# Kernel optimization log

Measured on AMD Instinct MI355X. Metric: run time of the kernel, lower is better.

## Reference

```python
import jax, jax.numpy as jnp
import numpy as np

B = 8192   # batch
S = 115    # state dim (fixed by slice layout)
E = 3072   # retrieval embed dim
C = 128    # compressed context dim
A = 23     # action dim
NE = 4096  # number of hyperedge keys
K = 10     # top-k retrieval
TAU = 1.0  # gumbel temperature
EPS = 1e-5 # layernorm eps


def _ln(x, g, b):
    m = x.mean(-1, keepdims=True)
    v = x.var(-1, keepdims=True)
    return (x - m) * jax.lax.rsqrt(v + EPS) * g + b


def _actor(ctx, extra, w1, b1, g1, be1, w2, b2, g2, be2, w3, b3):
    x = jnp.concatenate([ctx, extra], -1)
    x = jax.nn.relu(_ln(x @ w1 + b1, g1, be1))
    x = jax.nn.relu(_ln(x @ w2 + b2, g2, be2))
    return x @ w3 + b3


def setup_inputs() -> dict:
    key = jax.random.key(0)
    ks = iter(jax.random.split(key, 80))

    def W(shape):
        return jax.random.normal(next(ks), shape, jnp.float32) * (1.0 / float(np.sqrt(shape[0])))

    inp = {}
    inp["state"] = jax.random.normal(next(ks), (B, S), jnp.float32)
    u = jax.random.uniform(next(ks), (B, 4), jnp.float32, 1e-6, 1.0 - 1e-6)
    inp["gumbel_noise"] = -jnp.log(-jnp.log(u))  # standard Gumbel samples
    inp["keys"] = jax.random.normal(next(ks), (NE, E), jnp.float32)
    # state encoder 115 -> 512 -> 512 -> 3072 + LN
    inp["se_w1"] = W((S, 512)); inp["se_b1"] = jnp.zeros(512)
    inp["se_w2"] = W((512, 512)); inp["se_b2"] = jnp.zeros(512)
    inp["se_w3"] = W((512, E)); inp["se_b3"] = jnp.zeros(E)
    inp["se_g"] = jnp.ones(E); inp["se_beta"] = jnp.zeros(E)
    # context compressor 3072 -> 512 -> 128 + LN
    inp["cc_w1"] = W((E, 512)); inp["cc_b1"] = jnp.zeros(512)
    inp["cc_w2"] = W((512, C)); inp["cc_b2"] = jnp.zeros(C)
    inp["cc_g"] = jnp.ones(C); inp["cc_beta"] = jnp.zeros(C)
    # 4 actor experts, differing only in extra-slice width
    for p, e in [("a_pre", 50), ("a_scene", 20), ("a_effect", 10), ("a_rule", 15)]:
        inp[p + "_w1"] = W((C + e, C)); inp[p + "_b1"] = jnp.zeros(C)
        inp[p + "_g1"] = jnp.ones(C); inp[p + "_be1"] = jnp.zeros(C)
        inp[p + "_w2"] = W((C, C)); inp[p + "_b2"] = jnp.zeros(C)
        inp[p + "_g2"] = jnp.ones(C); inp[p + "_be2"] = jnp.zeros(C)
        inp[p + "_w3"] = W((C, A)) * 0.01; inp[p + "_b3"] = jnp.zeros(A)  # orthogonal gain=0.01 approx
    # gumbel router 115 -> 64 -> 64 -> 4
    inp["r_w1"] = W((S, 64)); inp["r_b1"] = jnp.zeros(64)
    inp["r_w2"] = W((64, 64)); inp["r_b2"] = jnp.zeros(64)
    inp["r_w3"] = W((64, 4)); inp["r_b3"] = jnp.zeros(4)
    # critic 115 -> 256 -> 256 -> 1
    inp["c_w1"] = W((S, 256)); inp["c_b1"] = jnp.zeros(256)
    inp["c_w2"] = W((256, 256)); inp["c_b2"] = jnp.zeros(256)
    inp["c_w3"] = W((256, 1)); inp["c_b3"] = jnp.zeros(1)
    return inp


def reference(state, gumbel_noise, keys, se_w1, se_b1, se_w2, se_b2, se_w3, se_b3, se_g, se_beta, cc_w1, cc_b1, cc_w2, cc_b2, cc_g, cc_beta, a_pre_w1, a_pre_b1, a_pre_g1, a_pre_be1, a_pre_w2, a_pre_b2, a_pre_g2, a_pre_be2, a_pre_w3, a_pre_b3, a_scene_w1, a_scene_b1, a_scene_g1, a_scene_be1, a_scene_w2, a_scene_b2, a_scene_g2, a_scene_be2, a_scene_w3, a_scene_b3, a_effect_w1, a_effect_b1, a_effect_g1, a_effect_be1, a_effect_w2, a_effect_b2, a_effect_g2, a_effect_be2, a_effect_w3, a_effect_b3, a_rule_w1, a_rule_b1, a_rule_g1, a_rule_be1, a_rule_w2, a_rule_b2, a_rule_g2, a_rule_be2, a_rule_w3, a_rule_b3, r_w1, r_b1, r_w2, r_b2, r_w3, r_b3, c_w1, c_b1, c_w2, c_b2, c_w3, c_b3):
    # 1) state -> query (StateEncoder)
    q = jax.nn.relu(state @ se_w1 + se_b1)
    q = jax.nn.relu(q @ se_w2 + se_b2)
    q = _ln(q @ se_w3 + se_b3, se_g, se_beta)  # (B, E)
    # 2) top-k hard retrieval from hypergraph memory (cosine sim)
    qn = q * jax.lax.rsqrt(jnp.sum(q * q, -1, keepdims=True) + 1e-12)
    kn = keys * jax.lax.rsqrt(jnp.sum(keys * keys, -1, keepdims=True) + 1e-12)
    scores = qn @ kn.T                          # (B, NE)
    _, idx = jax.lax.top_k(scores, K)           # (B, K)
    context = jnp.take(keys, idx, axis=0).mean(1)  # (B, E) mean-pool top-k raw embeddings
    # 3) compress to shared knowledge
    h = jax.nn.relu(context @ cc_w1 + cc_b1)
    shared = _ln(h @ cc_w2 + cc_b2, cc_g, cc_beta)  # (B, C)
    # 4) state slices + 4 actor experts
    belief = state[:, :50]
    location = state[:, 20:40]
    hp = state[:, 40:50]
    inv = state[:, 45:60]
    lp = _actor(shared, belief, a_pre_w1, a_pre_b1, a_pre_g1, a_pre_be1, a_pre_w2, a_pre_b2, a_pre_g2, a_pre_be2, a_pre_w3, a_pre_b3)
    ls = _actor(shared, location, a_scene_w1, a_scene_b1, a_scene_g1, a_scene_be1, a_scene_w2, a_scene_b2, a_scene_g2, a_scene_be2, a_scene_w3, a_scene_b3)
    le = _actor(shared, hp, a_effect_w1, a_effect_b1, a_effect_g1, a_effect_be1, a_effect_w2, a_effect_b2, a_effect_g2, a_effect_be2, a_effect_w3, a_effect_b3)
    lr = _actor(shared, inv, a_rule_w1, a_rule_b1, a_rule_g1, a_rule_be1, a_rule_w2, a_rule_b2, a_rule_g2, a_rule_be2, a_rule_w3, a_rule_b3)
    # 5) gumbel-softmax hard router (straight-through)
    rh = jax.nn.relu(state @ r_w1 + r_b1)
    rh = jax.nn.relu(rh @ r_w2 + r_b2)
    rl = jnp.clip(rh @ r_w3 + r_b3, -20.0, 20.0)
    y_soft = jax.nn.softmax((rl + gumbel_noise) / TAU, -1)
    y_hard = jax.nn.one_hot(jnp.argmax(y_soft, -1), 4, dtype=y_soft.dtype)
    alpha = y_soft + jax.lax.stop_gradient(y_hard - y_soft)  # (B, 4)
    # 6) combine expert logits
    all_l = jnp.stack([lp, ls, le, lr], 1)      # (B, 4, A)
    logits = jnp.einsum('bk,bka->ba', alpha, all_l)
    # critic value
    v = jax.nn.relu(state @ c_w1 + c_b1)
    v = jax.nn.relu(v @ c_w2 + c_b2)
    value = v @ c_w3 + c_b3                      # (B, 1)
    return (logits, alpha, value)
```

## Files before the change

### kernel.cpp

```cpp
#include <hip/hip_runtime.h>

constexpr int Bz = 8192;
constexpr int Sz = 115;
constexpr int Ez = 3072;
constexpr int NEz = 4096;

typedef __attribute__((ext_vector_type(8))) short short8;
typedef __attribute__((ext_vector_type(4))) float floatx4;
typedef unsigned short ushort_t;
typedef unsigned int uint_t;

__device__ __forceinline__ ushort_t f2bf(float f) {
  uint_t u = __float_as_uint(f);
  uint_t r = (u + 0x7FFFu + ((u >> 16) & 1u)) >> 16;
  return (ushort_t)r;
}
__device__ __forceinline__ float bf2f(ushort_t b) {
  uint_t u = ((uint_t)b) << 16;
  return __uint_as_float(u);
}
__device__ __forceinline__ ushort_t f2key(float v) {
  _Float16 h = (_Float16)v;
  ushort_t b = __builtin_bit_cast(ushort_t, h);
  return b ^ ((b & 0x8000u) ? 0xFFFFu : 0x8000u);
}
__device__ __forceinline__ uint_t umax_(uint_t a, uint_t b) { return a > b ? a : b; }

__device__ __forceinline__ void gload16(const ushort_t* g, ushort_t* l) {
  __builtin_amdgcn_global_load_lds(
      (__attribute__((address_space(1))) const void*)g,
      (__attribute__((address_space(3))) void*)l, 16, 0, 0);
}

template<bool RELU, bool BIAS>
__global__ __launch_bounds__(256)
void gemm128(const float* __restrict__ A, const float* __restrict__ Bm,
             const float* __restrict__ bias, float* __restrict__ C,
             int N, int Kd)
{
  __shared__ float As[16][132];
  __shared__ float Bs[16][132];
  const int t  = threadIdx.x;
  const int tx = t & 15, ty = t >> 4;
  const int row0 = blockIdx.y * 128;
  const int col0 = blockIdx.x * 128;
  const int ar = t >> 2, ac = (t & 3) * 4;
  const int bk = t >> 5, bc = (t & 31) * 4;
  const bool a4 = (Kd & 3) == 0;

  float acc[8][8];
#pragma unroll
  for (int i = 0; i < 8; ++i)
#pragma unroll
    for (int j = 0; j < 8; ++j) acc[i][j] = 0.f;

  for (int k0 = 0; k0 < Kd; k0 += 16) {
    const bool fullA = (k0 + 16 <= Kd) && a4;
    {
      const float* ap = A + (size_t)(row0 + ar) * Kd + k0 + ac;
      if (fullA) {
        float4 v0 = *(const float4*)ap;
        float4 v1 = *(const float4*)(ap + (size_t)64 * Kd);
        As[ac + 0][ar] = v0.x; As[ac + 1][ar] = v0.y;
        As[ac + 2][ar] = v0.z; As[ac + 3][ar] = v0.w;
        As[ac + 0][ar + 64] = v1.x; As[ac + 1][ar + 64] = v1.y;
        As[ac + 2][ar + 64] = v1.z; As[ac + 3][ar + 64] = v1.w;
      } else {
#pragma unroll
        for (int e = 0; e < 4; ++e) {
          const int k = k0 + ac + e;
          float v0 = 0.f, v1 = 0.f;
          if (k < Kd) { v0 = ap[e]; v1 = ap[e + (size_t)64 * Kd]; }
          As[ac + e][ar] = v0; As[ac + e][ar + 64] = v1;
        }
      }
    }
    {
      const float* bp = Bm + (size_t)(k0 + bk) * N + col0 + bc;
      if (k0 + 16 <= Kd) {
        *(float4*)&Bs[bk][bc]     = *(const float4*)bp;
        *(float4*)&Bs[bk + 8][bc] = *(const float4*)(bp + (size_t)8 * N);
      } else {
        float4 z; z.x = z.y = z.z = z.w = 0.f;
        *(float4*)&Bs[bk][bc]     = (k0 + bk     < Kd) ? *(const float4*)bp : z;
        *(float4*)&Bs[bk + 8][bc] = (k0 + bk + 8 < Kd) ? *(const float4*)(bp + (size_t)8 * N) : z;
      }
    }
    __syncthreads();
#pragma unroll
    for (int kk = 0; kk < 16; ++kk) {
      float a[8], b[8];
      *(float4*)&a[0] = *(const float4*)&As[kk][ty * 4];
      *(float4*)&a[4] = *(const float4*)&As[kk][64 + ty * 4];
      *(float4*)&b[0] = *(const float4*)&Bs[kk][tx * 4];
      *(float4*)&b[4] = *(const float4*)&Bs[kk][64 + tx * 4];
#pragma unroll
      for (int i = 0; i < 8; ++i)
#pragma unroll
        for (int j = 0; j < 8; ++j)
          acc[i][j] = fmaf(a[i], b[j], acc[i][j]);
    }
    __syncthreads();
  }

  float bv[8];
#pragma unroll
  for (int j = 0; j < 8; ++j) bv[j] = 0.f;
  if (BIAS) {
    *(float4*)&bv[0] = *(const float4*)&bias[col0 + tx * 4];
    *(float4*)&bv[4] = *(const float4*)&bias[col0 + 64 + tx * 4];
  }
#pragma unroll
  for (int i = 0; i < 8; ++i) {
    const int r = row0 + ((i < 4) ? (ty * 4 + i) : (64 + ty * 4 + i - 4));
    float o[8];
#pragma unroll
    for (int j = 0; j < 8; ++j) {
      o[j] = acc[i][j] + bv[j];
      if (RELU) o[j] = fmaxf(o[j], 0.f);
    }
    *(float4*)&C[(size_t)r * N + col0 + tx * 4]      = *(float4*)&o[0];
    *(float4*)&C[(size_t)r * N + col0 + 64 + tx * 4] = *(float4*)&o[4];
  }
}

struct GPart {
  const float* A; const float* Bm; const float* bias;
  float* C; ushort_t* Ch; ushort_t* Cl;
  int N; int Kd; int nbx;
};

__global__ __launch_bounds__(256)
void gemm128_dual(GPart g0, GPart g1)
{
  __shared__ float As[16][132];
  __shared__ float Bs[16][132];
  const int t  = threadIdx.x;
  const int tx = t & 15, ty = t >> 4;
  const bool p0 = (int)blockIdx.x < g0.nbx;
  GPart g = p0 ? g0 : g1;
  const int bx = p0 ? blockIdx.x : (blockIdx.x - g0.nbx);
  const int row0 = blockIdx.y * 128;
  const int col0 = bx * 128;
  const int Kd = g.Kd, N = g.N;
  const int ar = t >> 2, ac = (t & 3) * 4;
  const int bk = t >> 5, bc = (t & 31) * 4;
  const bool a4 = (Kd & 3) == 0;

  float acc[8][8];
#pragma unroll
  for (int i = 0; i < 8; ++i)
#pragma unroll
    for (int j = 0; j < 8; ++j) acc[i][j] = 0.f;

  for (int k0 = 0; k0 < Kd; k0 += 16) {
    const bool fullA = (k0 + 16 <= Kd) && a4;
    {
      const float* ap = g.A + (size_t)(row0 + ar) * Kd + k0 + ac;
      if (fullA) {
        float4 v0 = *(const float4*)ap;
        float4 v1 = *(const float4*)(ap + (size_t)64 * Kd);
        As[ac + 0][ar] = v0.x; As[ac + 1][ar] = v0.y;
        As[ac + 2][ar] = v0.z; As[ac + 3][ar] = v0.w;
        As[ac + 0][ar + 64] = v1.x; As[ac + 1][ar + 64] = v1.y;
        As[ac + 2][ar + 64] = v1.z; As[ac + 3][ar + 64] = v1.w;
      } else {
#pragma unroll
        for (int e = 0; e < 4; ++e) {
          const int k = k0 + ac + e;
          float v0 = 0.f, v1 = 0.f;
          if (k < Kd) { v0 = ap[e]; v1 = ap[e + (size_t)64 * Kd]; }
          As[ac + e][ar] = v0; As[ac + e][ar + 64] = v1;
        }
      }
    }
    {
      const float* bp = g.Bm + (size_t)(k0 + bk) * N + col0 + bc;
      if (k0 + 16 <= Kd) {
        *(float4*)&Bs[bk][bc]     = *(const float4*)bp;
        *(float4*)&Bs[bk + 8][bc] = *(const float4*)(bp + (size_t)8 * N);
      } else {
        float4 z; z.x = z.y = z.z = z.w = 0.f;
        *(float4*)&Bs[bk][bc]     = (k0 + bk     < Kd) ? *(const float4*)bp : z;
        *(float4*)&Bs[bk + 8][bc] = (k0 + bk + 8 < Kd) ? *(const float4*)(bp + (size_t)8 * N) : z;
      }
    }
    __syncthreads();
#pragma unroll
    for (int kk = 0; kk < 16; ++kk) {
      float a[8], b[8];
      *(float4*)&a[0] = *(const float4*)&As[kk][ty * 4];
      *(float4*)&a[4] = *(const float4*)&As[kk][64 + ty * 4];
      *(float4*)&b[0] = *(const float4*)&Bs[kk][tx * 4];
      *(float4*)&b[4] = *(const float4*)&Bs[kk][64 + tx * 4];
#pragma unroll
      for (int i = 0; i < 8; ++i)
#pragma unroll
        for (int j = 0; j < 8; ++j)
          acc[i][j] = fmaf(a[i], b[j], acc[i][j]);
    }
    __syncthreads();
  }

  float bv[8];
  *(float4*)&bv[0] = *(const float4*)&g.bias[col0 + tx * 4];
  *(float4*)&bv[4] = *(const float4*)&g.bias[col0 + 64 + tx * 4];
#pragma unroll
  for (int i = 0; i < 8; ++i) {
    const int r = row0 + ((i < 4) ? (ty * 4 + i) : (64 + ty * 4 + i - 4));
    float o[8];
#pragma unroll
    for (int j = 0; j < 8; ++j) o[j] = fmaxf(acc[i][j] + bv[j], 0.f);
    const size_t i0 = (size_t)r * N + col0 + tx * 4;
    const size_t i1 = i0 + 64;
    *(float4*)&g.C[i0] = *(float4*)&o[0];
    *(float4*)&g.C[i1] = *(float4*)&o[4];
    if (g.Ch) {
      ushort4 h0, l0, h1, l1;
      h0.x = f2bf(o[0]); l0.x = f2bf(o[0] - bf2f(h0.x));
      h0.y = f2bf(o[1]); l0.y = f2bf(o[1] - bf2f(h0.y));
      h0.z = f2bf(o[2]); l0.z = f2bf(o[2] - bf2f(h0.z));
      h0.w = f2bf(o[3]); l0.w = f2bf(o[3] - bf2f(h0.w));
      h1.x = f2bf(o[4]); l1.x = f2bf(o[4] - bf2f(h1.x));
      h1.y = f2bf(o[5]); l1.y = f2bf(o[5] - bf2f(h1.y));
      h1.z = f2bf(o[6]); l1.z = f2bf(o[6] - bf2f(h1.z));
      h1.w = f2bf(o[7]); l1.w = f2bf(o[7] - bf2f(h1.w));
      *(ushort4*)&g.Ch[i0] = h0; *(ushort4*)&g.Cl[i0] = l0;
      *(ushort4*)&g.Ch[i1] = h1; *(ushort4*)&g.Cl[i1] = l1;
    }
  }
}

template<int EPI>
__global__ __launch_bounds__(256)
void mfma_bt(const ushort_t* __restrict__ A, const ushort_t* __restrict__ B,
             const float* __restrict__ bias, void* __restrict__ Cout,
             int N, int Kd)
{
  __shared__ ushort_t Al[2 * 128 * 32];
  __shared__ ushort_t Bl[2 * 128 * 32];
  const int t = threadIdx.x;
  const int wid = t >> 6, lane = t & 63;
  const int wr = wid >> 1, wc = wid & 1;
  const int row0 = blockIdx.y << 7;
  const int col0 = blockIdx.x << 7;
  const int srow = lane >> 2;
  const int scol = (lane & 3) * 8;

  const ushort_t* ga0 = A + (size_t)(row0 + wid * 16 + srow) * Kd + scol;
  const ushort_t* ga1 = A + (size_t)(row0 + (wid + 4) * 16 + srow) * Kd + scol;
  const ushort_t* gb0 = B + (size_t)(col0 + wid * 16 + srow) * Kd + scol;
  const ushort_t* gb1 = B + (size_t)(col0 + (wid + 4) * 16 + srow) * Kd + scol;
  ushort_t* la0 = &Al[wid * 512];
  ushort_t* la1 = &Al[(wid + 4) * 512];
  ushort_t* lb0 = &Bl[wid * 512];
  ushort_t* lb1 = &Bl[(wid + 4) * 512];

  const int mr = lane & 15, qd = lane >> 4;

  floatx4 acc[4][4];
#pragma unroll
  for (int i = 0; i < 4; ++i)
#pragma unroll
    for (int j = 0; j < 4; ++j) acc[i][j] = (floatx4){0.f, 0.f, 0.f, 0.f};

  for (int kb = 0; kb < Kd; kb += 64) {
#pragma unroll
    for (int tt = 0; tt < 2; ++tt) {
      const int ko = kb + 32 * tt;
      const int lo = tt * 4096;
      gload16(ga0 + ko, la0 + lo);
      gload16(ga1 + ko, la1 + lo);
      gload16(gb0 + ko, lb0 + lo);
      gload16(gb1 + ko, lb1 + lo);
    }
    __syncthreads();
#pragma unroll
    for (int tt = 0; tt < 2; ++tt) {
      const int lo = tt * 4096;
      short8 aF[4], bF[4];
#pragma unroll
      for (int i = 0; i < 4; ++i)
        aF[i] = *(const short8*)&Al[lo + (wr * 64 + i * 16 + mr) * 32 + qd * 8];
#pragma unroll
      for (int j = 0; j < 4; ++j)
        bF[j] = *(const short8*)&Bl[lo + (wc * 64 + j * 16 + mr) * 32 + qd * 8];
#pragma unroll
      for (int i = 0; i < 4; ++i)
#pragma unroll
        for (int j = 0; j < 4; ++j)
          acc[i][j] = __builtin_amdgcn_mfma_f32_16x16x32_bf16(aF[i], bF[j], acc[i][j], 0, 0, 0);
    }
    __syncthreads();
  }

#pragma unroll
  for (int i = 0; i < 4; ++i) {
#pragma unroll
    for (int j = 0; j < 4; ++j) {
      const int col = col0 + wc * 64 + j * 16 + mr;
#pragma unroll
      for (int r = 0; r < 4; ++r) {
        const int row = row0 + wr * 64 + i * 16 + qd * 4 + r;
        if (EPI == 0) {
          ((ushort_t*)Cout)[(size_t)row * N + col] = f2key(acc[i][j][r]);
        } else {
          float v = acc[i][j][r] + bias[col];
          ((float*)Cout)[(size_t)row * N + col] = fmaxf(v, 0.f);
        }
      }
    }
  }
}

__global__ __launch_bounds__(256)
void mfma3_bt(const ushort_t* __restrict__ Ah, const ushort_t* __restrict__ Alo,
              const ushort_t* __restrict__ Bh, const ushort_t* __restrict__ Blo,
              const float* __restrict__ bias, float* __restrict__ Cout,
              int N, int Kd)
{
  __shared__ ushort_t AhL[128 * 32];
  __shared__ ushort_t AlL[128 * 32];
  __shared__ ushort_t BhL[128 * 32];
  __shared__ ushort_t BlL[128 * 32];
  const int t = threadIdx.x;
  const int wid = t >> 6, lane = t & 63;
  const int wr = wid >> 1, wc = wid & 1;
  const int row0 = blockIdx.y * 128;
  const int col0 = blockIdx.x * 128;
  const int srow = lane >> 2;
  const int scol = (lane & 3) * 8;

  const size_t aoff0 = (size_t)(row0 + wid * 16 + srow) * Kd + scol;
  const size_t aoff1 = (size_t)(row0 + (wid + 4) * 16 + srow) * Kd + scol;
  const size_t boff0 = (size_t)(col0 + wid * 16 + srow) * Kd + scol;
  const size_t boff1 = (size_t)(col0 + (wid + 4) * 16 + srow) * Kd + scol;
  const int l0 = (wid * 16) * 32;
  const int l1 = ((wid + 4) * 16) * 32;

  const int mr = lane & 15, qd = lane >> 4;

  floatx4 acc[4][4];
#pragma unroll
  for (int i = 0; i < 4; ++i)
#pragma unroll
    for (int j = 0; j < 4; ++j) acc[i][j] = (floatx4){0.f, 0.f, 0.f, 0.f};

  for (int kb = 0; kb < Kd; kb += 32) {
    gload16(Ah + aoff0 + kb, &AhL[l0]);
    gload16(Ah + aoff1 + kb, &AhL[l1]);
    gload16(Alo + aoff0 + kb, &AlL[l0]);
    gload16(Alo + aoff1 + kb, &AlL[l1]);
    gload16(Bh + boff0 + kb, &BhL[l0]);
    gload16(Bh + boff1 + kb, &BhL[l1]);
    gload16(Blo + boff0 + kb, &BlL[l0]);
    gload16(Blo + boff1 + kb, &BlL[l1]);
    __syncthreads();
    short8 ahF[4], alF[4], bhF[4], blF[4];
#pragma unroll
    for (int i = 0; i < 4; ++i) {
      const int o = (wr * 64 + i * 16 + mr) * 32 + qd * 8;
      ahF[i] = *(const short8*)&AhL[o];
      alF[i] = *(const short8*)&AlL[o];
    }
#pragma unroll
    for (int j = 0; j < 4; ++j) {
      const int o = (wc * 64 + j * 16 + mr) * 32 + qd * 8;
      bhF[j] = *(const short8*)&BhL[o];
      blF[j] = *(const short8*)&BlL[o];
    }
#pragma unroll
    for (int i = 0; i < 4; ++i)
#pragma unroll
      for (int j = 0; j < 4; ++j) {
        acc[i][j] = __builtin_amdgcn_mfma_f32_16x16x32_bf16(alF[i], bhF[j], acc[i][j], 0, 0, 0);
        acc[i][j] = __builtin_amdgcn_mfma_f32_16x16x32_bf16(ahF[i], blF[j], acc[i][j], 0, 0, 0);
        acc[i][j] = __builtin_amdgcn_mfma_f32_16x16x32_bf16(ahF[i], bhF[j], acc[i][j], 0, 0, 0);
      }
    __syncthreads();
  }

#pragma unroll
  for (int i = 0; i < 4; ++i) {
#pragma unroll
    for (int j = 0; j < 4; ++j) {
      const int col = col0 + wc * 64 + j * 16 + mr;
#pragma unroll
      for (int r = 0; r < 4; ++r) {
        const int row = row0 + wr * 64 + i * 16 + qd * 4 + r;
        Cout[(size_t)row * N + col] = acc[i][j][r] + bias[col];
      }
    }
  }
}

__global__ __launch_bounds__(256)
void gemm_scores(const float* __restrict__ A, const float* __restrict__ Bm,
                 const float* __restrict__ rk, ushort_t* __restrict__ S)
{
  __shared__ float As[16][132];
  __shared__ float Bs[16][132];
  const int t  = threadIdx.x;
  const int tx = t & 15, ty = t >> 4;
  const int row0 = blockIdx.y * 128;
  const int col0 = blockIdx.x * 128;
  const int ar = t >> 2, ac = (t & 3) * 4;
  const int Kd = Ez;

  float acc[8][8];
#pragma unroll
  for (int i = 0; i < 8; ++i)
#pragma unroll
    for (int j = 0; j < 8; ++j) acc[i][j] = 0.f;

  for (int k0 = 0; k0 < Kd; k0 += 16) {
    {
      const float* ap = A + (size_t)(row0 + ar) * Kd + k0 + ac;
      float4 v0 = *(const float4*)ap;
      float4 v1 = *(const float4*)(ap + (size_t)64 * Kd);
      As[ac + 0][ar] = v0.x; As[ac + 1][ar] = v0.y;
      As[ac + 2][ar] = v0.z; As[ac + 3][ar] = v0.w;
      As[ac + 0][ar + 64] = v1.x; As[ac + 1][ar + 64] = v1.y;
      As[ac + 2][ar + 64] = v1.z; As[ac + 3][ar + 64] = v1.w;
    }
    {
      const float* bp = Bm + (size_t)(col0 + ar) * Kd + k0 + ac;
      float4 v0 = *(const float4*)bp;
      float4 v1 = *(const float4*)(bp + (size_t)64 * Kd);
      Bs[ac + 0][ar] = v0.x; Bs[ac + 1][ar] = v0.y;
      Bs[ac + 2][ar] = v0.z; Bs[ac + 3][ar] = v0.w;
      Bs[ac + 0][ar + 64] = v1.x; Bs[ac + 1][ar + 64] = v1.y;
      Bs[ac + 2][ar + 64] = v1.z; Bs[ac + 3][ar + 64] = v1.w;
    }
    __syncthreads();
#pragma unroll
    for (int kk = 0; kk < 16; ++kk) {
      float a[8], b[8];
      *(float4*)&a[0] = *(const float4*)&As[kk][ty * 4];
      *(float4*)&a[4] = *(const float4*)&As[kk][64 + ty * 4];
      *(float4*)&b[0] = *(const float4*)&Bs[kk][tx * 4];
      *(float4*)&b[4] = *(const float4*)&Bs[kk][64 + tx * 4];
#pragma unroll
      for (int i = 0; i < 8; ++i)
#pragma unroll
        for (int j = 0; j < 8; ++j)
          acc[i][j] = fmaf(a[i], b[j], acc[i][j]);
    }
    __syncthreads();
  }

  float rk0[8];
  *(float4*)&rk0[0] = *(const float4*)&rk[col0 + tx * 4];
  *(float4*)&rk0[4] = *(const float4*)&rk[col0 + 64 + tx * 4];
#pragma unroll
  for (int i = 0; i < 8; ++i) {
    const int r = row0 + ((i < 4) ? (ty * 4 + i) : (64 + ty * 4 + i - 4));
    ushort4 h0, h1;
    h0.x = f2key(acc[i][0] * rk0[0]); h0.y = f2key(acc[i][1] * rk0[1]);
    h0.z = f2key(acc[i][2] * rk0[2]); h0.w = f2key(acc[i][3] * rk0[3]);
    h1.x = f2key(acc[i][4] * rk0[4]); h1.y = f2key(acc[i][5] * rk0[5]);
    h1.z = f2key(acc[i][6] * rk0[6]); h1.w = f2key(acc[i][7] * rk0[7]);
    *(ushort4*)&S[(size_t)r * NEz + col0 + tx * 4]      = h0;
    *(ushort4*)&S[(size_t)r * NEz + col0 + 64 + tx * 4] = h1;
  }
}

struct LN4 {
  const float* W[4]; const float* b[4]; const float* g[4]; const float* be[4];
  int eoff[4]; int elen[4];
};

template<bool RELU, bool HASEXT>
__global__ __launch_bounds__(256)
void gemm_ln4(const float* __restrict__ A1base, size_t a1stride, int K1,
              const float* __restrict__ A2, LN4 p,
              float* __restrict__ outbase, size_t ostride)
{
  __shared__ float As[32][68];
  __shared__ float Bs[32][132];
  __shared__ float rsum[64][17];
  __shared__ float rsq[64][17];
  __shared__ float stm[64], str[64];
  const int a = blockIdx.y;
  const float* A1 = A1base + (size_t)a * a1stride;
  float* out = outbase + (size_t)a * ostride;
  const float* W = p.W[a];
  const float* bias = p.b[a];
  const float* g = p.g[a];
  const float* be = p.be[a];
  const int eoff = HASEXT ? p.eoff[a] : 0;
  const int K2 = HASEXT ? p.elen[a] : 0;

  const int t = threadIdx.x;
  const int tx = t & 15, ty = t >> 4;
  const int row0 = blockIdx.x * 64;
  const int Kt = K1 + K2;
  const int ar = t >> 2, ac = (t & 3) * 8;
  const int bk = t >> 3, bc = (t & 7) * 16;

  float acc[4][8];
#pragma unroll
  for (int i = 0; i < 4; ++i)
#pragma unroll
    for (int j = 0; j < 8; ++j) acc[i][j] = 0.f;

  for (int k0 = 0; k0 < Kt; k0 += 32) {
    const int grow = row0 + ar;
#pragma unroll
    for (int e = 0; e < 8; ++e) {
      const int k = k0 + ac + e;
      float v = 0.f;
      if (k < K1)      v = A1[(size_t)grow * K1 + k];
      else if (k < Kt) v = A2[(size_t)grow * 115 + eoff + (k - K1)];
      As[ac + e][ar] = v;
    }
    {
      const int k = k0 + bk;
#pragma unroll
      for (int qd = 0; qd < 4; ++qd) {
        float4 z; z.x = z.y = z.z = z.w = 0.f;
        *(float4*)&Bs[bk][bc + 4 * qd] =
            (k < Kt) ? *(const float4*)&W[(size_t)k * 128 + bc + 4 * qd] : z;
      }
    }
    __syncthreads();
#pragma unroll
    for (int kk = 0; kk < 32; ++kk) {
      float av[4], bv2[8];
      *(float4*)&av[0]  = *(const float4*)&As[kk][ty * 4];
      *(float4*)&bv2[0] = *(const float4*)&Bs[kk][tx * 4];
      *(float4*)&bv2[4] = *(const float4*)&Bs[kk][64 + tx * 4];
#pragma unroll
      for (int i = 0; i < 4; ++i)
#pragma unroll
        for (int j = 0; j < 8; ++j)
          acc[i][j] = fmaf(av[i], bv2[j], acc[i][j]);
    }
    __syncthreads();
  }

  float bv[8];
  *(float4*)&bv[0] = *(const float4*)&bias[tx * 4];
  *(float4*)&bv[4] = *(const float4*)&bias[64 + tx * 4];
#pragma unroll
  for (int i = 0; i < 4; ++i) {
    float s = 0.f, q = 0.f;
#pragma unroll
    for (int j = 0; j < 8; ++j) {
      acc[i][j] += bv[j];
      s += acc[i][j];
      q += acc[i][j] * acc[i][j];
    }
    rsum[ty * 4 + i][tx] = s;
    rsq[ty * 4 + i][tx]  = q;
  }
  __syncthreads();
  if (t < 64) {
    float s = 0.f, q = 0.f;
#pragma unroll
    for (int x = 0; x < 16; ++x) { s += rsum[t][x]; q += rsq[t][x]; }
    const float m = s * (1.f / 128.f);
    const float v = q * (1.f / 128.f) - m * m;
    stm[t] = m;
    str[t] = rsqrtf(v + 1e-5f);
  }
  __syncthreads();
#pragma unroll
  for (int i = 0; i < 4; ++i) {
    const int r = ty * 4 + i;
    const float m = stm[r], rs = str[r];
    float o[8];
#pragma unroll
    for (int j = 0; j < 8; ++j) {
      const int col = (j < 4) ? (tx * 4 + j) : (64 + tx * 4 + (j - 4));
      float y = (acc[i][j] - m) * rs * g[col] + be[col];
      if (RELU) y = fmaxf(y, 0.f);
      o[j] = y;
    }
    *(float4*)&out[(size_t)(row0 + r) * 128 + tx * 4]      = *(float4*)&o[0];
    *(float4*)&out[(size_t)(row0 + r) * 128 + 64 + tx * 4] = *(float4*)&o[4];
  }
}

__device__ __forceinline__ float blockSum256(float v, float* sh)
{
#pragma unroll
  for (int d = 32; d; d >>= 1) v += __shfl_down(v, d, 64);
  __syncthreads();
  if ((threadIdx.x & 63) == 0) sh[threadIdx.x >> 6] = v;
  __syncthreads();
  return sh[0] + sh[1] + sh[2] + sh[3];
}

template<bool CVT>
__global__ __launch_bounds__(256)
void ln_l2_q(float* __restrict__ q, const float* __restrict__ g,
             const float* __restrict__ be, ushort_t* __restrict__ qb)
{
  __shared__ float sh[4];
  const int row = blockIdx.x, t = threadIdx.x;
  float* qr = q + (size_t)row * Ez;
  float x[12];
#pragma unroll
  for (int i = 0; i < 12; ++i) x[i] = qr[t + (i << 8)];
  float s = 0.f;
#pragma unroll
  for (int i = 0; i < 12; ++i) s += x[i];
  const float m = blockSum256(s, sh) * (1.f / (float)Ez);
  float vs = 0.f;
#pragma unroll
  for (int i = 0; i < 12; ++i) { const float d = x[i] - m; vs += d * d; }
  const float v = blockSum256(vs, sh) * (1.f / (float)Ez);
  const float rs = rsqrtf(v + 1e-5f);
  float y[12]; float qs = 0.f;
#pragma unroll
  for (int i = 0; i < 12; ++i) {
    const int c = t + (i << 8);
    const float yy = (x[i] - m) * rs * g[c] + be[c];
    y[i] = yy; qs += yy * yy;
  }
  const float tot = blockSum256(qs, sh);
  const float s2 = rsqrtf(tot + 1e-12f);
#pragma unroll
  for (int i = 0; i < 12; ++i) {
    const int c = t + (i << 8);
    const float yn = y[i] * s2;
    qr[c] = yn;
    if (CVT) qb[(size_t)row * Ez + c] = f2bf(yn);
  }
}

__global__ __launch_bounds__(256)
void keynorm(const float* __restrict__ keys, float* __restrict__ rk)
{
  __shared__ float sh[4];
  const int row = blockIdx.x, t = threadIdx.x;
  const float* xr = keys + (size_t)row * Ez;
  float qs = 0.f;
#pragma unroll
  for (int i = 0; i < 12; ++i) { const float x = xr[t + (i << 8)]; qs += x * x; }
  const float tot = blockSum256(qs, sh);
  if (t == 0) rk[row] = rsqrtf(tot + 1e-12f);
}

__global__ __launch_bounds__(256)
void keys_norm_cvt(const float* __restrict__ keys, float* __restrict__ rk,
                   ushort_t* __restrict__ knb)
{
  __shared__ float sh[4];
  const int row = blockIdx.x, t = threadIdx.x;
  const float* xr = keys + (size_t)row * Ez;
  float x[12]; float qs = 0.f;
#pragma unroll
  for (int i = 0; i < 12; ++i) { x[i] = xr[t + (i << 8)]; qs += x[i] * x[i]; }
  const float tot = blockSum256(qs, sh);
  const float s = rsqrtf(tot + 1e-12f);
  if (t == 0) rk[row] = s;
#pragma unroll
  for (int i = 0; i < 12; ++i)
    knb[(size_t)row * Ez + t + (i << 8)] = f2bf(x[i] * s);
}

__global__ __launch_bounds__(256)
void w3_transpose_split(const float* __restrict__ w,
                        ushort_t* __restrict__ hT, ushort_t* __restrict__ lT)
{
  __shared__ float tile[64][65];
  const int k0 = blockIdx.x * 64;
  const int n0 = blockIdx.y * 64;
  const int t = threadIdx.x;
  const int c = t & 63, r4 = t >> 6;
#pragma unroll
  for (int rr = 0; rr < 16; ++rr) {
    const int r = rr * 4 + r4;
    tile[r][c] = w[(size_t)(k0 + r) * 3072 + n0 + c];
  }
  __syncthreads();
#pragma unroll
  for (int rr = 0; rr < 16; ++rr) {
    const int n = rr * 4 + r4;
    const float a = tile[c][n];
    const ushort_t h = f2bf(a);
    hT[(size_t)(n0 + n) * 512 + k0 + c] = h;
    lT[(size_t)(n0 + n) * 512 + k0 + c] = f2bf(a - bf2f(h));
  }
}

__global__ __launch_bounds__(256)
void cvt_w1t_t(const float* __restrict__ w, ushort_t* __restrict__ out)
{
  __shared__ float tile[64][65];
  const int k0 = blockIdx.x * 64;
  const int n0 = blockIdx.y * 64;
  const int t = threadIdx.x;
  const int c = t & 63, r4 = t >> 6;
#pragma unroll
  for (int rr = 0; rr < 16; ++rr) {
    const int r = rr * 4 + r4;
    tile[r][c] = w[(size_t)(k0 + r) * 512 + n0 + c];
  }
  __syncthreads();
#pragma unroll
  for (int rr = 0; rr < 16; ++rr) {
    const int n = rr * 4 + r4;
    out[(size_t)(n0 + n) * Ez + k0 + c] = f2bf(tile[c][n]);
  }
}

__global__ __launch_bounds__(256)
void topk16(const ushort_t* __restrict__ S, int* __restrict__ outIdx)
{
  __shared__ uint_t cand[64];
  const int row = blockIdx.x, t = threadIdx.x;
  const int w = t >> 6, lane = t & 63;
  const int base = (w << 10) + (lane << 4);
  const ushort_t* sr = S + (size_t)row * NEz + base;
  uint4 v0 = *(const uint4*)sr;
  uint4 v1 = *(const uint4*)(sr + 8);
  const uint_t cb = (uint_t)(4095 - base);
  uint_t p[16];
  p[0]  = ((v0.x & 0xFFFFu) << 12) | (cb - 0);
  p[1]  = ((v0.x >> 16)     << 12) | (cb - 1);
  p[2]  = ((v0.y & 0xFFFFu) << 12) | (cb - 2);
  p[3]  = ((v0.y >> 16)     << 12) | (cb - 3);
  p[4]  = ((v0.z & 0xFFFFu) << 12) | (cb - 4);
  p[5]  = ((v0.z >> 16)     << 12) | (cb - 5);
  p[6]  = ((v0.w & 0xFFFFu) << 12) | (cb - 6);
  p[7]  = ((v0.w >> 16)     << 12) | (cb - 7);
  p[8]  = ((v1.x & 0xFFFFu) << 12) | (cb - 8);
  p[9]  = ((v1.x >> 16)     << 12) | (cb - 9);
  p[10] = ((v1.y & 0xFFFFu) << 12) | (cb - 10);
  p[11] = ((v1.y >> 16)     << 12) | (cb - 11);
  p[12] = ((v1.z & 0xFFFFu) << 12) | (cb - 12);
  p[13] = ((v1.z >> 16)     << 12) | (cb - 13);
  p[14] = ((v1.w & 0xFFFFu) << 12) | (cb - 14);
  p[15] = ((v1.w >> 16)     << 12) | (cb - 15);

  for (int it = 0; it < 16; ++it) {
    uint_t m = p[0];
#pragma unroll
    for (int j = 1; j < 16; ++j) m = umax_(m, p[j]);
#pragma unroll
    for (int d = 1; d < 64; d <<= 1)
      m = umax_(m, (uint_t)__shfl_xor((int)m, d, 64));
    if (lane == it) cand[(w << 4) + it] = m;
#pragma unroll
    for (int j = 0; j < 16; ++j) p[j] = (p[j] == m) ? 0u : p[j];
  }
  __syncthreads();
  if (t < 64) {
    uint_t mine = cand[t];
    for (int it = 0; it < 16; ++it) {
      uint_t m = mine;
#pragma unroll
      for (int d = 1; d < 64; d <<= 1)
        m = umax_(m, (uint_t)__shfl_xor((int)m, d, 64));
      if (t == it) outIdx[(size_t)row * 16 + it] = 4095 - (int)(m & 0xFFFu);
      mine = (mine == m) ? 0u : mine;
    }
  }
}

template<bool BFOUT>
__global__ __launch_bounds__(256)
void rescore_gather(const float* __restrict__ qn, const float* __restrict__ keys,
                    const float* __restrict__ rk, const int* __restrict__ cand,
                    void* __restrict__ ctxOut)
{
  __shared__ float qs[Ez];
  __shared__ double sv[16];
  __shared__ int si[16];
  __shared__ int sel10[10];
  const int row = blockIdx.x, t = threadIdx.x;
  const int w = t >> 6, lane = t & 63;

  {
    const float* qr = qn + (size_t)row * Ez;
#pragma unroll
    for (int i = 0; i < 3; ++i) {
      const int c = (t << 2) + (i << 10);
      *(float4*)&qs[c] = *(const float4*)&qr[c];
    }
  }
  __syncthreads();

#pragma unroll
  for (int cc = 0; cc < 4; ++cc) {
    const int slot = w * 4 + cc;
    const int id = cand[(size_t)row * 16 + slot];
    const float* kr = keys + (size_t)id * Ez;
    double s = 0.0;
#pragma unroll
    for (int it = 0; it < 12; ++it) {
      const int c = (lane << 2) + (it << 8);
      float4 k4 = *(const float4*)&kr[c];
      float4 q4 = *(const float4*)&qs[c];
      s += (double)q4.x * (double)k4.x;
      s += (double)q4.y * (double)k4.y;
      s += (double)q4.z * (double)k4.z;
      s += (double)q4.w * (double)k4.w;
    }
#pragma unroll
    for (int d = 32; d; d >>= 1) s += __shfl_down(s, d, 64);
    if (lane == 0) { sv[slot] = s * (double)rk[id]; si[slot] = id; }
  }
  __syncthreads();

  if (t == 0) {
    for (int it = 0; it < 10; ++it) {
      int bj = 0; double bvv = sv[0]; int bi = si[0];
      for (int j = 1; j < 16; ++j) {
        const double v = sv[j]; const int i2 = si[j];
        if (v > bvv || (v == bvv && i2 < bi)) { bj = j; bvv = v; bi = i2; }
      }
      sel10[it] = bi;
      sv[bj] = -1e300;
    }
  }
  __syncthreads();

  int id[10];
#pragma unroll
  for (int j = 0; j < 10; ++j) id[j] = sel10[j];

#pragma unroll
  for (int i = 0; i < 3; ++i) {
    const int c = (t << 2) + (i << 10);
    float4 a = {0.f, 0.f, 0.f, 0.f};
#pragma unroll
    for (int j = 0; j < 10; ++j) {
      float4 v = *(const float4*)&keys[(size_t)id[j] * Ez + c];
      a.x += v.x; a.y += v.y; a.z += v.z; a.w += v.w;
    }
    if (BFOUT) {
      ushort4 o;
      o.x = f2bf(a.x * 0.1f); o.y = f2bf(a.y * 0.1f);
      o.z = f2bf(a.z * 0.1f); o.w = f2bf(a.w * 0.1f);
      *(ushort4*)&((ushort_t*)ctxOut)[(size_t)row * Ez + c] = o;
    } else {
      float4 o;
      o.x = a.x * 0.1f; o.y = a.y * 0.1f; o.z = a.z * 0.1f; o.w = a.w * 0.1f;
      *(float4*)&((float*)ctxOut)[(size_t)row * Ez + c] = o;
    }
  }
}

__global__ __launch_bounds__(256)
void router_kernel(const float* __restrict__ state, const float* __restrict__ gn,
                   const float* __restrict__ w1, const float* __restrict__ b1,
                   const float* __restrict__ w2, const float* __restrict__ b2,
                   const float* __restrict__ w3, const float* __restrict__ b3,
                   float* __restrict__ outAlpha)
{
  const int row = blockIdx.x * 256 + threadIdx.x;
  const float* sr = state + (size_t)row * Sz;
  float h1[64];
#pragma unroll
  for (int j = 0; j < 64; ++j) h1[j] = b1[j];
  for (int k = 0; k < Sz; ++k) {
    const float a = sr[k];
    const float* wr = w1 + (size_t)k * 64;
#pragma unroll
    for (int j = 0; j < 64; ++j) h1[j] = fmaf(a, wr[j], h1[j]);
  }
#pragma unroll
  for (int j = 0; j < 64; ++j) h1[j] = fmaxf(h1[j], 0.f);
  float h2[64];
#pragma unroll
  for (int j = 0; j < 64; ++j) h2[j] = b2[j];
#pragma unroll
  for (int k = 0; k < 64; ++k) {
    const float a = h1[k];
    const float* wr = w2 + (size_t)k * 64;
#pragma unroll
    for (int j = 0; j < 64; ++j) h2[j] = fmaf(a, wr[j], h2[j]);
  }
#pragma unroll
  for (int j = 0; j < 64; ++j) h2[j] = fmaxf(h2[j], 0.f);
  float z[4];
#pragma unroll
  for (int a = 0; a < 4; ++a) {
    float s = b3[a];
#pragma unroll
    for (int k = 0; k < 64; ++k) s = fmaf(h2[k], w3[k * 4 + a], s);
    s = fminf(fmaxf(s, -20.f), 20.f);
    z[a] = s + gn[(size_t)row * 4 + a];
  }
  float mz = z[0];
#pragma unroll
  for (int a = 1; a < 4; ++a) mz = fmaxf(mz, z[a]);
  float e[4]; float se = 0.f;
#pragma unroll
  for (int a = 0; a < 4; ++a) { e[a] = expf(z[a] - mz); se += e[a]; }
  const float inv = 1.f / se;
  float y[4];
#pragma unroll
  for (int a = 0; a < 4; ++a) y[a] = e[a] * inv;
  int am = 0;
#pragma unroll
  for (int a = 1; a < 4; ++a) if (y[a] > y[am]) am = a;
#pragma unroll
  for (int a = 0; a < 4; ++a) {
    const float hard = (a == am) ? 1.f : 0.f;
    outAlpha[(size_t)row * 4 + a] = y[a] + (hard - y[a]);
  }
}

__global__ __launch_bounds__(256)
void critic_head(const float* __restrict__ c2, const float* __restrict__ w3,
                 const float* __restrict__ b3, float* __restrict__ outv)
{
  const int row = blockIdx.x * 256 + threadIdx.x;
  const float* xr = c2 + (size_t)row * 256;
  float s = b3[0];
  for (int k = 0; k < 256; ++k) s = fmaf(xr[k], w3[k], s);
  outv[row] = s;
}

struct HeadP { const float* w3[4]; const float* b3[4]; };

__global__ __launch_bounds__(256)
void actor_head4(const float* __restrict__ x2g, HeadP p,
                 const float* __restrict__ alpha, float* __restrict__ outL)
{
  __shared__ float wsm[4][128 * 23];
  __shared__ float bs[4][23];
  const int t = threadIdx.x;
#pragma unroll
  for (int a = 0; a < 4; ++a) {
    for (int i = t; i < 128 * 23; i += 256) wsm[a][i] = p.w3[a][i];
    if (t < 23) bs[a][t] = p.b3[a][t];
  }
  __syncthreads();
  const int row = blockIdx.x * 32 + (t >> 3);
  const int cg = t & 7;
  float sum[3] = {0.f, 0.f, 0.f};
#pragma unroll
  for (int a = 0; a < 4; ++a) {
    const float al = alpha[(size_t)row * 4 + a];
    const float* xr = x2g + (size_t)a * Bz * 128 + (size_t)row * 128;
    float acc[3] = {0.f, 0.f, 0.f};
    for (int kk = 0; kk < 128; ++kk) {
      const float xa = xr[kk];
#pragma unroll
      for (int j = 0; j < 3; ++j) {
        const int col = cg + 8 * j;
        if (col < 23) acc[j] = fmaf(xa, wsm[a][kk * 23 + col], acc[j]);
      }
    }
#pragma unroll
    for (int j = 0; j < 3; ++j) {
      const int col = cg + 8 * j;
      if (col < 23) sum[j] += al * (acc[j] + bs[a][col]);
    }
  }
#pragma unroll
  for (int j = 0; j < 3; ++j) {
    const int col = cg + 8 * j;
    if (col < 23) outL[(size_t)row * 23 + col] = sum[j];
  }
}

extern "C" void kernel_launch(void* const* d_in, const int* in_sizes, int n_in,
                              void* d_out, int out_size, void* d_ws, size_t ws_size,
                              hipStream_t stream)
{
  const float* state  = (const float*)d_in[0];
  const float* gumbel = (const float*)d_in[1];
  const float* keys   = (const float*)d_in[2];
  const float* se_w1 = (const float*)d_in[3];
  const float* se_b1 = (const float*)d_in[4];
  const float* se_w2 = (const float*)d_in[5];
  const float* se_b2 = (const float*)d_in[6];
  const float* se_w3 = (const float*)d_in[7];
  const float* se_b3 = (const float*)d_in[8];
  const float* se_g  = (const float*)d_in[9];
  const float* se_be = (const float*)d_in[10];
  const float* cc_w1 = (const float*)d_in[11];
  const float* cc_b1 = (const float*)d_in[12];
  const float* cc_w2 = (const float*)d_in[13];
  const float* cc_b2 = (const float*)d_in[14];
  const float* cc_g  = (const float*)d_in[15];
  const float* cc_be = (const float*)d_in[16];
  const float* r_w1 = (const float*)d_in[57];
  const float* r_b1 = (const float*)d_in[58];
  const float* r_w2 = (const float*)d_in[59];
  const float* r_b2 = (const float*)d_in[60];
  const float* r_w3 = (const float*)d_in[61];
  const float* r_b3 = (const float*)d_in[62];
  const float* c_w1 = (const float*)d_in[63];
  const float* c_b1 = (const float*)d_in[64];
  const float* c_w2 = (const float*)d_in[65];
  const float* c_b2 = (const float*)d_in[66];
  const float* c_w3 = (const float*)d_in[67];
  const float* c_b3 = (const float*)d_in[68];

  float* wsf = (float*)d_ws;
  const size_t qF = (size_t)Bz * Ez;
  const size_t uF = (size_t)16777216;
  float* q = wsf;
  float* U = wsf + qF;
  float* sA  = U;
  float* sB  = U + 4194304;
  ushort_t* sBh  = (ushort_t*)(U + 8388608);
  ushort_t* sBl  = (ushort_t*)(U + 10485760);
  ushort_t* w3hT = (ushort_t*)(U + 12582912);
  ushort_t* w3lT = (ushort_t*)(U + 14155776);
  ushort_t* scoresU = (ushort_t*)U;
  float* shr = U;
  float* x1g = U + 1 * 1048576;
  float* x2g = U + 5 * 1048576;
  float* cch = U + 9 * 1048576;
  float* cr1 = q;
  float* cr2 = q + 2097152;
  ushort_t* qbf  = (ushort_t*)(wsf + qF + uF);
  ushort_t* knbf = qbf + qF;
  ushort_t* w1T  = knbf + (size_t)NEz * Ez;
  const size_t bfHalves = qF + (size_t)NEz * Ez + (size_t)512 * Ez;
  const size_t baseBytes = (qF + uF) * sizeof(float);
  const size_t tailBytes = 4096 * 4 + (size_t)Bz * 16 * 4;
  const bool fast = ws_size >= baseBytes + bfHalves * 2 + tailBytes;
  float* tailF = (float*)((char*)d_ws + (fast ? baseBytes + bfHalves * 2 : baseBytes));
  float* rk  = tailF;
  int* cand  = (int*)(tailF + 4096);
  ushort_t* ctxb = (ushort_t*)q;

  float* outL = (float*)d_out;
  float* outA = outL + (size_t)Bz * 23;
  float* outV = outA + (size_t)Bz * 4;

  const dim3 blk(256);

  {
    GPart e0 = {state, se_w1, se_b1, sA, nullptr, nullptr, 512, 115, 4};
    GPart e1 = {state, c_w1,  c_b1,  cr1, nullptr, nullptr, 256, 115, 2};
    gemm128_dual<<<dim3(6, 64), blk, 0, stream>>>(e0, e1);
  }
  {
    GPart f0 = {sA, se_w2, se_b2, sB, fast ? sBh : nullptr, fast ? sBl : nullptr,
                512, 512, 4};
    GPart f1 = {cr1, c_w2, c_b2, cr2, nullptr, nullptr, 256, 256, 2};
    gemm128_dual<<<dim3(6, 64), blk, 0, stream>>>(f0, f1);
  }
  critic_head<<<dim3(32), blk, 0, stream>>>(cr2, c_w3, c_b3, outV);
  router_kernel<<<dim3(32), blk, 0, stream>>>(state, gumbel, r_w1, r_b1, r_w2, r_b2,
                                              r_w3, r_b3, outA);

  if (fast) {
    w3_transpose_split<<<dim3(8, 48), blk, 0, stream>>>(se_w3, w3hT, w3lT);
    mfma3_bt<<<dim3(24, 64), blk, 0, stream>>>(sBh, sBl, w3hT, w3lT, se_b3, q, 3072, 512);
    ln_l2_q<true><<<dim3(Bz), blk, 0, stream>>>(q, se_g, se_be, qbf);
    keys_norm_cvt<<<dim3(NEz), blk, 0, stream>>>(keys, rk, knbf);
    cvt_w1t_t<<<dim3(48, 8), blk, 0, stream>>>(cc_w1, w1T);
    mfma_bt<0><<<dim3(32, 64), blk, 0, stream>>>(qbf, knbf, nullptr, scoresU, NEz, Ez);
  } else {
    gemm128<false, true><<<dim3(24, 64), blk, 0, stream>>>(sB, se_w3, se_b3, q, 3072, 512);
    ln_l2_q<false><<<dim3(Bz), blk, 0, stream>>>(q, se_g, se_be, nullptr);
    keynorm<<<dim3(NEz), blk, 0, stream>>>(keys, rk);
    gemm_scores<<<dim3(32, 64), blk, 0, stream>>>(q, keys, rk, scoresU);
  }

  topk16<<<dim3(Bz), blk, 0, stream>>>(scoresU, cand);

  if (fast) {
    rescore_gather<true><<<dim3(Bz), blk, 0, stream>>>(q, keys, rk, cand, ctxb);
    mfma_bt<1><<<dim3(4, 64), blk, 0, stream>>>(ctxb, w1T, cc_b1, cch, 512, Ez);
  } else {
    rescore_gather<false><<<dim3(Bz), blk, 0, stream>>>(q, keys, rk, cand, q);
    gemm128<true, true><<<dim3(4, 64), blk, 0, stream>>>(q, cc_w1, cc_b1, cch, 512, Ez);
  }
  {
    LN4 pcc = {};
    pcc.W[0] = cc_w2; pcc.b[0] = cc_b2; pcc.g[0] = cc_g; pcc.be[0] = cc_be;
    gemm_ln4<false, false><<<dim3(128, 1), blk, 0, stream>>>(cch, 0, 512, nullptr, pcc,
                                                             shr, 0);
  }

  {
    LN4 p1 = {}, p2 = {};
    HeadP ph = {};
    const int eoffs[4] = {0, 20, 40, 45};
    const int elens[4] = {50, 20, 10, 15};
    for (int a = 0; a < 4; ++a) {
      const int base = 17 + 10 * a;
      p1.W[a]  = (const float*)d_in[base + 0];
      p1.b[a]  = (const float*)d_in[base + 1];
      p1.g[a]  = (const float*)d_in[base + 2];
      p1.be[a] = (const float*)d_in[base + 3];
      p1.eoff[a] = eoffs[a]; p1.elen[a] = elens[a];
      p2.W[a]  = (const float*)d_in[base + 4];
      p2.b[a]  = (const float*)d_in[base + 5];
      p2.g[a]  = (const float*)d_in[base + 6];
      p2.be[a] = (const float*)d_in[base + 7];
      ph.w3[a] = (const float*)d_in[base + 8];
      ph.b3[a] = (const float*)d_in[base + 9];
    }
    gemm_ln4<true, true ><<<dim3(128, 4), blk, 0, stream>>>(shr, 0, 128, state, p1,
                                                            x1g, (size_t)Bz * 128);
    gemm_ln4<true, false><<<dim3(128, 4), blk, 0, stream>>>(x1g, (size_t)Bz * 128, 128,
                                                            nullptr, p2,
                                                            x2g, (size_t)Bz * 128);
    actor_head4<<<dim3(256), blk, 0, stream>>>(x2g, ph, outA, outL);
  }
}
```

Baseline: 1.325 ms.

## Move state-encoder layer 2 to split-bf16 MFMA and retune retrieval GEMMs

The second state-encoder layer now runs as a 3-pass split-bf16 MFMA GEMM. The first layer writes hi/lo bf16 halves directly instead of fp32, so the fp32 intermediate is no longer stored. The scores GEMM stages three 32-wide K sub-tiles per sync instead of two, and the context-compressor GEMM uses a new 64-row tile kernel that launches more blocks. The critic head is rewritten as a wave-parallel dot product with shuffle reductions, and the critic's second layer runs as a separate GEMM. Together these add launches and workspace aliasing changes that need to stay consistent.

Measured after the change: 1.312 ms. Within noise of the previous version (-1.0%).

```diff
diff --git a/kernel.cpp b/kernel.cpp
--- a/kernel.cpp
+++ b/kernel.cpp
@@ -213,8 +213,10 @@
     for (int j = 0; j < 8; ++j) o[j] = fmaxf(acc[i][j] + bv[j], 0.f);
     const size_t i0 = (size_t)r * N + col0 + tx * 4;
     const size_t i1 = i0 + 64;
-    *(float4*)&g.C[i0] = *(float4*)&o[0];
-    *(float4*)&g.C[i1] = *(float4*)&o[4];
+    if (g.C) {
+      *(float4*)&g.C[i0] = *(float4*)&o[0];
+      *(float4*)&g.C[i1] = *(float4*)&o[4];
+    }
     if (g.Ch) {
       ushort4 h0, l0, h1, l1;
       h0.x = f2bf(o[0]); l0.x = f2bf(o[0] - bf2f(h0.x));
@@ -231,14 +233,13 @@
   }
 }
 
-template<int EPI>
+template<int NSUB>
 __global__ __launch_bounds__(256)
 void mfma_bt(const ushort_t* __restrict__ A, const ushort_t* __restrict__ B,
-             const float* __restrict__ bias, void* __restrict__ Cout,
-             int N, int Kd)
-{
-  __shared__ ushort_t Al[2 * 128 * 32];
-  __shared__ ushort_t Bl[2 * 128 * 32];
+             ushort_t* __restrict__ Cout, int N, int Kd)
+{
+  __shared__ ushort_t Al[NSUB * 4096];
+  __shared__ ushort_t Bl[NSUB * 4096];
   const int t = threadIdx.x;
   const int wid = t >> 6, lane = t & 63;
   const int wr = wid >> 1, wc = wid & 1;
@@ -264,9 +265,9 @@
 #pragma unroll
     for (int j = 0; j < 4; ++j) acc[i][j] = (floatx4){0.f, 0.f, 0.f, 0.f};
 
-  for (int kb = 0; kb < Kd; kb += 64) {
-#pragma unroll
-    for (int tt = 0; tt < 2; ++tt) {
+  for (int kb = 0; kb < Kd; kb += 32 * NSUB) {
+#pragma unroll
+    for (int tt = 0; tt < NSUB; ++tt) {
       const int ko = kb + 32 * tt;
       const int lo = tt * 4096;
       gload16(ga0 + ko, la0 + lo);
@@ -276,7 +277,7 @@
     }
     __syncthreads();
 #pragma unroll
-    for (int tt = 0; tt < 2; ++tt) {
+    for (int tt = 0; tt < NSUB; ++tt) {
       const int lo = tt * 4096;
       short8 aF[4], bF[4];
 #pragma unroll
@@ -302,21 +303,18 @@
 #pragma unroll
       for (int r = 0; r < 4; ++r) {
         const int row = row0 + wr * 64 + i * 16 + qd * 4 + r;
-        if (EPI == 0) {
-          ((ushort_t*)Cout)[(size_t)row * N + col] = f2key(acc[i][j][r]);
-        } else {
-          float v = acc[i][j][r] + bias[col];
-          ((float*)Cout)[(size_t)row * N + col] = fmaxf(v, 0.f);
-        }
+        Cout[(size_t)row * N + col] = f2key(acc[i][j][r]);
       }
     }
   }
 }
 
+template<int EPI>
 __global__ __launch_bounds__(256)
 void mfma3_bt(const ushort_t* __restrict__ Ah, const ushort_t* __restrict__ Alo,
               const ushort_t* __restrict__ Bh, const ushort_t* __restrict__ Blo,
               const float* __restrict__ bias, float* __restrict__ Cout,
+              ushort_t* __restrict__ Ch, ushort_t* __restrict__ Cl,
               int N, int Kd)
 {
   __shared__ ushort_t AhL[128 * 32];
@@ -388,7 +386,88 @@
 #pragma unroll
       for (int r = 0; r < 4; ++r) {
         const int row = row0 + wr * 64 + i * 16 + qd * 4 + r;
-        Cout[(size_t)row * N + col] = acc[i][j][r] + bias[col];
+        const float v = acc[i][j][r] + bias[col];
+        if (EPI == 0) {
+          Cout[(size_t)row * N + col] = v;
+        } else {
+          const float y = fmaxf(v, 0.f);
+          const ushort_t h = f2bf(y);
+          Ch[(size_t)row * N + col] = h;
+          Cl[(size_t)row * N + col] = f2bf(y - bf2f(h));
+        }
+      }
+    }
+  }
+}
+
+__global__ __launch_bounds__(256)
+void mfma_bt64(const ushort_t* __restrict__ A, const ushort_t* __restrict__ B,
+               const float* __restrict__ bias, float* __restrict__ Cout,
+               int N, int Kd)
+{
+  __shared__ ushort_t Al[2 * 64 * 32];
+  __shared__ ushort_t Bl[2 * 128 * 32];
+  const int t = threadIdx.x;
+  const int wid = t >> 6, lane = t & 63;
+  const int row0 = blockIdx.y << 6;
+  const int col0 = blockIdx.x << 7;
+  const int srow = lane >> 2;
+  const int scol = (lane & 3) * 8;
+  const int mr = lane & 15, qd = lane >> 4;
+
+  const ushort_t* gsrc[6];
+  ushort_t* ldst[6];
+#pragma unroll
+  for (int m = 0; m < 6; ++m) {
+    const int c = wid * 6 + m;
+    if (c < 8) {
+      const int sub = c >> 2, grp = c & 3;
+      gsrc[m] = A + (size_t)(row0 + grp * 16 + srow) * Kd + sub * 32 + scol;
+      ldst[m] = &Al[sub * 2048 + (grp * 16 + srow) * 32];
+    } else {
+      const int b = c - 8, sub = b >> 3, grp = b & 7;
+      gsrc[m] = B + (size_t)(col0 + grp * 16 + srow) * Kd + sub * 32 + scol;
+      ldst[m] = &Bl[sub * 4096 + (grp * 16 + srow) * 32];
+    }
+  }
+
+  floatx4 acc[4][2];
+#pragma unroll
+  for (int i = 0; i < 4; ++i)
+#pragma unroll
+    for (int j = 0; j < 2; ++j) acc[i][j] = (floatx4){0.f, 0.f, 0.f, 0.f};
+
+  for (int kb = 0; kb < Kd; kb += 64) {
+#pragma unroll
+    for (int m = 0; m < 6; ++m) gload16(gsrc[m] + kb, ldst[m]);
+    __syncthreads();
+#pragma unroll
+    for (int sub = 0; sub < 2; ++sub) {
+      short8 aF[4], bF[2];
+#pragma unroll
+      for (int i = 0; i < 4; ++i)
+        aF[i] = *(const short8*)&Al[sub * 2048 + (i * 16 + mr) * 32 + qd * 8];
+#pragma unroll
+      for (int j = 0; j < 2; ++j)
+        bF[j] = *(const short8*)&Bl[sub * 4096 + (wid * 32 + j * 16 + mr) * 32 + qd * 8];
+#pragma unroll
+      for (int i = 0; i < 4; ++i)
+#pragma unroll
+        for (int j = 0; j < 2; ++j)
+          acc[i][j] = __builtin_amdgcn_mfma_f32_16x16x32_bf16(aF[i], bF[j], acc[i][j], 0, 0, 0);
+    }
+    __syncthreads();
+  }
+
+#pragma unroll
+  for (int i = 0; i < 4; ++i) {
+#pragma unroll
+    for (int j = 0; j < 2; ++j) {
+      const int col = col0 + wid * 32 + j * 16 + mr;
+#pragma unroll
+      for (int r = 0; r < 4; ++r) {
+        const int row = row0 + i * 16 + qd * 4 + r;
+        Cout[(size_t)row * N + col] = fmaxf(acc[i][j][r] + bias[col], 0.f);
       }
     }
   }
@@ -662,8 +741,8 @@
 }
 
 __global__ __launch_bounds__(256)
-void w3_transpose_split(const float* __restrict__ w,
-                        ushort_t* __restrict__ hT, ushort_t* __restrict__ lT)
+void wt_split(const float* __restrict__ w, ushort_t* __restrict__ hT,
+              ushort_t* __restrict__ lT, int C)
 {
   __shared__ float tile[64][65];
   const int k0 = blockIdx.x * 64;
@@ -673,7 +752,7 @@
 #pragma unroll
   for (int rr = 0; rr < 16; ++rr) {
     const int r = rr * 4 + r4;
-    tile[r][c] = w[(size_t)(k0 + r) * 3072 + n0 + c];
+    tile[r][c] = w[(size_t)(k0 + r) * C + n0 + c];
   }
   __syncthreads();
 #pragma unroll
@@ -910,11 +989,21 @@
 void critic_head(const float* __restrict__ c2, const float* __restrict__ w3,
                  const float* __restrict__ b3, float* __restrict__ outv)
 {
-  const int row = blockIdx.x * 256 + threadIdx.x;
-  const float* xr = c2 + (size_t)row * 256;
-  float s = b3[0];
-  for (int k = 0; k < 256; ++k) s = fmaf(xr[k], w3[k], s);
-  outv[row] = s;
+  const int t = threadIdx.x;
+  const int w = t >> 6, lane = t & 63;
+  const int row0 = blockIdx.x * 64 + w * 16;
+  float wv[4];
+  *(float4*)&wv[0] = *(const float4*)&w3[lane * 4];
+  const float b0 = b3[0];
+#pragma unroll
+  for (int rr = 0; rr < 16; ++rr) {
+    const int row = row0 + rr;
+    float4 x = *(const float4*)&c2[(size_t)row * 256 + lane * 4];
+    float s = x.x * wv[0] + x.y * wv[1] + x.z * wv[2] + x.w * wv[3];
+#pragma unroll
+    for (int d = 32; d; d >>= 1) s += __shfl_down(s, d, 64);
+    if (lane == 0) outv[row] = s + b0;
+  }
 }
 
 struct HeadP { const float* w3[4]; const float* b3[4]; };
@@ -1000,17 +1089,22 @@
   const size_t uF = (size_t)16777216;
   float* q = wsf;
   float* U = wsf + qF;
-  float* sA  = U;
-  float* sB  = U + 4194304;
-  ushort_t* sBh  = (ushort_t*)(U + 8388608);
-  ushort_t* sBl  = (ushort_t*)(U + 10485760);
-  ushort_t* w3hT = (ushort_t*)(U + 12582912);
-  ushort_t* w3lT = (ushort_t*)(U + 14155776);
+  ushort_t* sAh  = (ushort_t*)(U + 0);
+  ushort_t* sAl  = (ushort_t*)(U + 2097152);
+  ushort_t* sBh  = (ushort_t*)(U + 4194304);
+  ushort_t* sBl  = (ushort_t*)(U + 6291456);
+  ushort_t* w3hT = (ushort_t*)(U + 8388608);
+  ushort_t* w3lT = (ushort_t*)(U + 9175040);
+  ushort_t* w2hT = (ushort_t*)(U + 9961472);
+  ushort_t* w2lT = (ushort_t*)(U + 10092544);
+  float* sA = U;
+  float* sB = U + 4194304;
   ushort_t* scoresU = (ushort_t*)U;
+  ushort_t* ctxb = (ushort_t*)U;
+  float* cch = U + 12582912;
   float* shr = U;
   float* x1g = U + 1 * 1048576;
   float* x2g = U + 5 * 1048576;
-  float* cch = U + 9 * 1048576;
   float* cr1 = q;
   float* cr2 = q + 2097152;
   ushort_t* qbf  = (ushort_t*)(wsf + qF + uF);
@@ -1023,7 +1117,6 @@
   float* tailF = (float*)((char*)d_ws + (fast ? baseBytes + bfHalves * 2 : baseBytes));
   float* rk  = tailF;
   int* cand  = (int*)(tailF + 4096);
-  ushort_t* ctxb = (ushort_t*)q;
 
   float* outL = (float*)d_out;
   float* outA = outL + (size_t)Bz * 23;
@@ -1032,27 +1125,33 @@
   const dim3 blk(256);
 
   {
-    GPart e0 = {state, se_w1, se_b1, sA, nullptr, nullptr, 512, 115, 4};
-    GPart e1 = {state, c_w1,  c_b1,  cr1, nullptr, nullptr, 256, 115, 2};
+    GPart e0 = {state, se_w1, se_b1, fast ? nullptr : sA,
+                fast ? sAh : nullptr, fast ? sAl : nullptr, 512, 115, 4};
+    GPart e1 = {state, c_w1, c_b1, cr1, nullptr, nullptr, 256, 115, 2};
     gemm128_dual<<<dim3(6, 64), blk, 0, stream>>>(e0, e1);
   }
-  {
-    GPart f0 = {sA, se_w2, se_b2, sB, fast ? sBh : nullptr, fast ? sBl : nullptr,
-                512, 512, 4};
-    GPart f1 = {cr1, c_w2, c_b2, cr2, nullptr, nullptr, 256, 256, 2};
-    gemm128_dual<<<dim3(6, 64), blk, 0, stream>>>(f0, f1);
-  }
-  critic_head<<<dim3(32), blk, 0, stream>>>(cr2, c_w3, c_b3, outV);
+  gemm128<true, true><<<dim3(2, 64), blk, 0, stream>>>(cr1, c_w2, c_b2, cr2, 256, 256);
+
+  if (fast) {
+    wt_split<<<dim3(8, 8),  blk, 0, stream>>>(se_w2, w2hT, w2lT, 512);
+    wt_split<<<dim3(8, 48), blk, 0, stream>>>(se_w3, w3hT, w3lT, 3072);
+    mfma3_bt<1><<<dim3(4, 64), blk, 0, stream>>>(sAh, sAl, w2hT, w2lT, se_b2,
+                                                 nullptr, sBh, sBl, 512, 512);
+  } else {
+    gemm128<true, true><<<dim3(4, 64), blk, 0, stream>>>(sA, se_w2, se_b2, sB, 512, 512);
+  }
+
+  critic_head<<<dim3(128), blk, 0, stream>>>(cr2, c_w3, c_b3, outV);
   router_kernel<<<dim3(32), blk, 0, stream>>>(state, gumbel, r_w1, r_b1, r_w2, r_b2,
                                               r_w3, r_b3, outA);
 
   if (fast) {
-    w3_transpose_split<<<dim3(8, 48), blk, 0, stream>>>(se_w3, w3hT, w3lT);
-    mfma3_bt<<<dim3(24, 64), blk, 0, stream>>>(sBh, sBl, w3hT, w3lT, se_b3, q, 3072, 512);
+    mfma3_bt<0><<<dim3(24, 64), blk, 0, stream>>>(sBh, sBl, w3hT, w3lT, se_b3,
+                                                  q, nullptr, nullptr, 3072, 512);
     ln_l2_q<true><<<dim3(Bz), blk, 0, stream>>>(q, se_g, se_be, qbf);
     keys_norm_cvt<<<dim3(NEz), blk, 0, stream>>>(keys, rk, knbf);
     cvt_w1t_t<<<dim3(48, 8), blk, 0, stream>>>(cc_w1, w1T);
-    mfma_bt<0><<<dim3(32, 64), blk, 0, stream>>>(qbf, knbf, nullptr, scoresU, NEz, Ez);
+    mfma_bt<3><<<dim3(32, 64), blk, 0, stream>>>(qbf, knbf, scoresU, NEz, Ez);
   } else {
     gemm128<false, true><<<dim3(24, 64), blk, 0, stream>>>(sB, se_w3, se_b3, q, 3072, 512);
     ln_l2_q<false><<<dim3(Bz), blk, 0, stream>>>(q, se_g, se_be, nullptr);
@@ -1064,7 +1163,7 @@
 
   if (fast) {
     rescore_gather<true><<<dim3(Bz), blk, 0, stream>>>(q, keys, rk, cand, ctxb);
-    mfma_bt<1><<<dim3(4, 64), blk, 0, stream>>>(ctxb, w1T, cc_b1, cch, 512, Ez);
+    mfma_bt64<<<dim3(4, 128), blk, 0, stream>>>(ctxb, w1T, cc_b1, cch, 512, Ez);
   } else {
     rescore_gather<false><<<dim3(Bz), blk, 0, stream>>>(q, keys, rk, cand, q);
     gemm128<true, true><<<dim3(4, 64), blk, 0, stream>>>(q, cc_w1, cc_b1, cch, 512, Ez);
```
